# Kernel optimization log

Measured on AMD Instinct MI355X. Metric: run time of the kernel, lower is better.

Reference implementation:

```python
import jax, jax.numpy as jnp
import numpy as np

T, B, N, D, H = 12, 32, 64, 2, 128
HID, HEAD = 32, 4          # GATBlock n_hid, n_head; HEAD*HID == H
M = N * (N - 1)            # edge rows per get_graph
N_ACT = N - 1              # active nodes per batch row


def _make_graph():
    rec = np.zeros((M, N), np.float32)
    snd = np.zeros((M, N), np.float32)
    k = np.arange(N_ACT * N_ACT)
    ii = np.repeat(np.arange(N_ACT), N_ACT)
    jj = np.tile(np.arange(N_ACT), N_ACT)
    snd[k, ii] = 1.0
    rec[k, jj] = 1.0
    return rec, snd


def setup_inputs() -> dict:
    key = jax.random.key(0)
    ks = jax.random.split(key, 16)
    rec, snd = _make_graph()
    inp = {
        "inputs": jax.random.normal(ks[0], (T, B, N, D), jnp.float32),
        "hidden": jax.random.normal(ks[1], (B, N, H), jnp.float32),
        "rel_rec": jnp.asarray(np.broadcast_to(rec, (B, M, N)).copy()),
        "rel_send": jnp.asarray(np.broadcast_to(snd, (B, M, N)).copy()),
        # GATBlock rn1: fc1(D->HID), fc2(2*HID->HEAD)
        "rn1_W1": jax.random.normal(ks[2], (HID, D)) * 0.1,
        "rn1_b1": jnp.zeros((HID,)),
        "rn1_W2": jax.random.normal(ks[3], (HEAD, 2 * HID)) * 0.1,
        "rn1_b2": jnp.zeros((HEAD,)),
        # GATBlock rn2: fc1(H->HID), fc2(2*HID->HEAD)
        "rn2_W1": jax.random.normal(ks[4], (HID, H)) * 0.1,
        "rn2_b1": jnp.zeros((HID,)),
        "rn2_W2": jax.random.normal(ks[5], (HEAD, 2 * HID)) * 0.1,
        "rn2_b2": jnp.zeros((HEAD,)),
        # GRUCell(H, H)
        "gru_Wih": jax.random.normal(ks[6], (3 * H, H)) * 0.05,
        "gru_Whh": jax.random.normal(ks[7], (3 * H, H)) * 0.05,
        "gru_bih": jnp.zeros((3 * H,)),
        "gru_bhh": jnp.zeros((3 * H,)),
        # out Linear(H, D)
        "out_W": jax.random.normal(ks[8], (D, H)) * 0.1,
        "out_b": jnp.zeros((D,)),
    }
    return inp


def _gat_block(x_in, rel_rec, rel_send, W1, b1, W2, b2):
    # x_in: B x N x Din
    x = x_in @ W1.T + b1                                   # B,N,HID
    s = jnp.einsum('bmn,bnd->bmd', rel_send, x)            # B,M,HID (senders)
    r = jnp.einsum('bmn,bnd->bmd', rel_rec, x)             # B,M,HID (receivers)
    a = jax.nn.elu(jnp.concatenate([s, r], -1) @ W2.T + b2)  # B,M,HEAD
    # per-receiving-node masked softmax over the edge dim (edge2node)
    m = rel_rec[..., None] > 0                             # B,M,N,1
    logits = jnp.where(m, a[:, :, None, :], -jnp.inf)      # B,M,N,HEAD
    mx = jnp.max(logits, axis=1, keepdims=True)
    mx = jnp.where(jnp.isfinite(mx), mx, 0.0)
    e = jnp.where(m, jnp.exp(logits - mx), 0.0)
    denom = jnp.sum(e, axis=1, keepdims=True)
    att = e / jnp.where(denom > 0, denom, 1.0)             # B,M,N,HEAD
    # weighted scatter-sum: outer(att_edge, sender_feat) summed per node
    out = jnp.einsum('bmnh,bmd->bnhd', att, s)             # B,N,HEAD,HID
    Bn, Nn = x_in.shape[0], x_in.shape[1]
    return jax.nn.elu(out.reshape(Bn, Nn, HEAD * HID))     # B,N,H


def _gru_cell(x, h, Wih, Whh, bih, bhh):
    gi = x @ Wih.T + bih
    gh = h @ Whh.T + bhh
    i_r, i_z, i_n = jnp.split(gi, 3, axis=-1)
    h_r, h_z, h_n = jnp.split(gh, 3, axis=-1)
    r = jax.nn.sigmoid(i_r + h_r)
    z = jax.nn.sigmoid(i_z + h_z)
    n = jnp.tanh(i_n + r * h_n)
    return (1.0 - z) * n + z * h


def reference(inputs, hidden, rel_rec, rel_send,
              rn1_W1, rn1_b1, rn1_W2, rn1_b2,
              rn2_W1, rn2_b1, rn2_W2, rn2_b2,
              gru_Wih, gru_Whh, gru_bih, gru_bhh,
              out_W, out_b):
    def step(h, x_t):
        x = _gat_block(x_t, rel_rec, rel_send, rn1_W1, rn1_b1, rn1_W2, rn1_b2)
        h = _gru_cell(x, h, gru_Wih, gru_Whh, gru_bih, gru_bhh)
        h = _gat_block(h, rel_rec, rel_send, rn2_W1, rn2_b1, rn2_W2, rn2_b2)
        return h, None
    h_final, _ = jax.lax.scan(step, hidden, inputs)
    pred = h_final @ out_W.T + out_b                       # B,N,D
    return pred
```

## Files before the change

kernel.cpp:

```cpp
#include <hip/hip_runtime.h>


#define T_   12
#define B_   32
#define N_   64
#define D_   2
#define H_   128
#define HID_ 32
#define HEAD_ 4
#define NA_  63

__device__ __forceinline__ float eluf(float x){ return x>0.f ? x : expm1f(x); }

#define OFF_H    0u
#define OFF_X1   262144u
#define OFF_PS1  1048576u
#define OFF_PR1  1146880u
#define OFF_XG   1245184u
#define OFF_X2   4390912u
#define OFF_PS2  4456448u
#define OFF_PR2  4464640u
#define OFF_WT   OFF_X1
#define OFF_GI   4472832u
#define WS_NEED_A ((4472832ull + 9437184ull) * 4ull)

__global__ void gat1_fc(const float* __restrict__ inp, const float* __restrict__ W1,
                        const float* __restrict__ b1, const float* __restrict__ W2,
                        const float* __restrict__ b2,
                        float* __restrict__ x1_all, float* __restrict__ ps_all,
                        float* __restrict__ pr_all){
  int grp = blockIdx.x;
  int tid = threadIdx.x;
  __shared__ float sx1[N_*HID_];
  __shared__ float sW1[HID_*D_];
  __shared__ float sb1[HID_];
  __shared__ float sW2[HEAD_*2*HID_];
  __shared__ float sxin[N_*D_];
  if(tid < 64)  sW1[tid] = W1[tid];
  if(tid < 32)  sb1[tid] = b1[tid];
  sW2[tid] = W2[tid];
  if(tid < 128) sxin[tid] = inp[grp*N_*D_ + tid];
  __syncthreads();
  for(int o = tid; o < N_*HID_; o += 256){
    int n = o >> 5, k = o & 31;
    float v = sb1[k] + sxin[n*2]*sW1[k*2] + sxin[n*2+1]*sW1[k*2+1];
    sx1[o] = v;
    x1_all[grp*N_*HID_ + o] = v;
  }
  __syncthreads();
  for(int p = tid; p < N_*8; p += 256){
    int n = p >> 3, q = p & 7, hh = q & 3;
    const float* w  = sW2 + hh*64 + ((q < 4) ? 0 : 32);
    const float* xr = sx1 + n*32;
    float acc = (q < 4) ? b2[hh] : 0.f;
    #pragma unroll
    for(int c = 0; c < 32; c++) acc += xr[c]*w[c];
    if(q < 4) ps_all[grp*N_*HEAD_ + n*4 + hh] = acc;
    else      pr_all[grp*N_*HEAD_ + n*4 + hh] = acc;
  }
}

__global__ void prep_wt(const float* __restrict__ Wih, const float* __restrict__ Whh,
                        float* __restrict__ wtb){
  int idx = blockIdx.x*256 + threadIdx.x;
  int k4 = idx / 768, j = idx - k4*768;
  const float* src = (j < 384) ? (Wih + (size_t)j*H_) : (Whh + (size_t)(j-384)*H_);
  ((float4*)wtb)[idx] = ((const float4*)src)[k4];
}

__global__ __launch_bounds__(256) void gat_att_gi(const float* __restrict__ x1,
    const float* __restrict__ ps, const float* __restrict__ pr,
    const float* __restrict__ wtb, float* __restrict__ gi){
  int blk = blockIdx.x, g = blk >> 1, ch = blk & 1, tid = threadIdx.x;
  __shared__ float sX[N_*HID_];
  __shared__ float sPs[N_*HEAD_];
  __shared__ float sPr[N_*HEAD_];
  __shared__ __align__(16) float sxg[N_][H_];
  {
    const float4* xs = (const float4*)(x1 + (size_t)g*(N_*HID_));
    ((float4*)sX)[tid]       = xs[tid];
    ((float4*)sX)[tid + 256] = xs[tid + 256];
    sPs[tid] = ps[g*(N_*HEAD_) + tid];
    sPr[tid] = pr[g*(N_*HEAD_) + tid];
  }
  __syncthreads();
  if(tid < NA_*HEAD_){
    int r = tid, hh = r & 3, j = r >> 2;
    float prv = sPr[r];
    float tmax = -1e30f;
    for(int i = 0; i < NA_; i++) tmax = fmaxf(tmax, sPs[i*4 + hh]);
    float m = eluf(tmax + prv);
    float4 acc[8];
    #pragma unroll
    for(int k = 0; k < 8; k++) acc[k] = make_float4(0.f,0.f,0.f,0.f);
    float s = 0.f;
    #pragma unroll 3
    for(int i = 0; i < NA_; i++){
      float tt = sPs[i*4 + hh] + prv;
      float v = tt > 0.f ? tt : expm1f(tt);
      float p = expf(v - m);
      s += p;
      const float4* sxp = (const float4*)&sX[i*32];
      #pragma unroll
      for(int k = 0; k < 8; k++){
        float4 xv = sxp[k];
        acc[k].x += p*xv.x; acc[k].y += p*xv.y;
        acc[k].z += p*xv.z; acc[k].w += p*xv.w;
      }
    }
    float inv = 1.f/s;
    float4* orow = (float4*)&sxg[j][hh*32];
    #pragma unroll
    for(int k = 0; k < 8; k++){
      float4 o;
      o.x = eluf(acc[k].x*inv); o.y = eluf(acc[k].y*inv);
      o.z = eluf(acc[k].z*inv); o.w = eluf(acc[k].w*inv);
      orow[k] = o;
    }
  } else {
    float4 z4 = make_float4(0.f,0.f,0.f,0.f);
    float4* zp = (float4*)sxg[NA_];
    for(int k = tid - NA_*HEAD_; k < 32; k += 4) zp[k] = z4;
  }
  __syncthreads();
  {
    int c = ch*64 + (tid & 63), rh8 = (tid >> 6) * 8;
    const float4* wt4 = (const float4*)wtb;
    #pragma unroll
    for(int pass = 0; pass < 2; pass++){
      int rbase = pass*32 + rh8;
      float ar[8]={0,0,0,0,0,0,0,0}, az[8]={0,0,0,0,0,0,0,0}, an[8]={0,0,0,0,0,0,0,0};
      #pragma unroll 2
      for(int k4 = 0; k4 < 32; k4++){
        float4 w0 = wt4[k4*768 + c];
        float4 w1 = wt4[k4*768 + 128 + c];
        float4 w2 = wt4[k4*768 + 256 + c];
        #pragma unroll
        for(int rr = 0; rr < 8; rr++){
          float4 xv = ((const float4*)sxg[rbase + rr])[k4];
          ar[rr] += w0.x*xv.x + w0.y*xv.y + w0.z*xv.z + w0.w*xv.w;
          az[rr] += w1.x*xv.x + w1.y*xv.y + w1.z*xv.z + w1.w*xv.w;
          an[rr] += w2.x*xv.x + w2.y*xv.y + w2.z*xv.z + w2.w*xv.w;
        }
      }
      #pragma unroll
      for(int rr = 0; rr < 8; rr++){
        size_t base = (size_t)(g*N_ + rbase + rr)*384;
        gi[base + c]       = ar[rr];
        gi[base + 128 + c] = az[rr];
        gi[base + 256 + c] = an[rr];
      }
    }
  }
}

__global__ __launch_bounds__(256) void gat_att_big2(const float* __restrict__ x1,
    const float* __restrict__ ps, const float* __restrict__ pr,
    float* __restrict__ out){
  int blk = blockIdx.x, g = blk >> 1, dh = blk & 1, tid = threadIdx.x;
  __shared__ float sX[N_*HID_];
  __shared__ float sPs[N_*HEAD_];
  __shared__ float sPr[N_*HEAD_];
  {
    const float4* xs = (const float4*)(x1 + (size_t)g*(N_*HID_));
    ((float4*)sX)[tid]       = xs[tid];
    ((float4*)sX)[tid + 256] = xs[tid + 256];
    sPs[tid] = ps[g*(N_*HEAD_) + tid];
    sPr[tid] = pr[g*(N_*HEAD_) + tid];
  }
  __syncthreads();
  float* outg = out + (size_t)g*(N_*H_);
  if(tid < NA_*HEAD_){
    int r = tid, hh = r & 3;
    float prv = sPr[r];
    float tmax = -1e30f;
    for(int i = 0; i < NA_; i++) tmax = fmaxf(tmax, sPs[i*4 + hh]);
    float m = eluf(tmax + prv);
    float4 acc[4];
    #pragma unroll
    for(int k = 0; k < 4; k++) acc[k] = make_float4(0.f,0.f,0.f,0.f);
    float s = 0.f;
    #pragma unroll 3
    for(int i = 0; i < NA_; i++){
      float tt = sPs[i*4 + hh] + prv;
      float v = tt > 0.f ? tt : expm1f(tt);
      float p = expf(v - m);
      s += p;
      const float4* sxp = (const float4*)&sX[i*32 + dh*16];
      #pragma unroll
      for(int k = 0; k < 4; k++){
        float4 xv = sxp[k];
        acc[k].x += p*xv.x; acc[k].y += p*xv.y;
        acc[k].z += p*xv.z; acc[k].w += p*xv.w;
      }
    }
    float inv = 1.f/s;
    float4* orow = (float4*)(outg + (r>>2)*H_ + hh*32 + dh*16);
    #pragma unroll
    for(int k = 0; k < 4; k++){
      float4 o;
      o.x = eluf(acc[k].x*inv); o.y = eluf(acc[k].y*inv);
      o.z = eluf(acc[k].z*inv); o.w = eluf(acc[k].w*inv);
      orow[k] = o;
    }
  } else {
    int hh = tid - NA_*HEAD_;
    float4 z4 = make_float4(0.f,0.f,0.f,0.f);
    float4* zp = (float4*)(outg + NA_*H_ + hh*32 + dh*16);
    zp[0]=z4; zp[1]=z4; zp[2]=z4; zp[3]=z4;
  }
}

__global__ __launch_bounds__(256) void gru_fc8(
    const float* __restrict__ gi, const float* __restrict__ hidden0, int t0,
    const float* __restrict__ x2prev, const float* __restrict__ psprev,
    const float* __restrict__ prprev,
    const float* __restrict__ wtb,
    const float* __restrict__ bih, const float* __restrict__ bhh,
    const float* __restrict__ W1, const float* __restrict__ b1,
    const float* __restrict__ W2, const float* __restrict__ b2,
    float* __restrict__ x2, float* __restrict__ ps2, float* __restrict__ pr2){
  int tid = threadIdx.x, blk = blockIdx.x;
  int g0 = blk*4, g = blk>>4, jbase = (blk&15)*4;
  __shared__ __align__(16) float sX[N_*HID_];
  __shared__ float sPs[N_*HEAD_];
  __shared__ __align__(16) float sh[4][H_];
  __shared__ __align__(16) float shn[4][H_];
  __shared__ float spart[2][12][H_];
  __shared__ float sx2[4][HID_];

  if(t0){
    if(tid < 128) ((float4*)sh)[tid] = ((const float4*)(hidden0 + (size_t)g0*H_))[tid];
  } else {
    ((float4*)sX)[tid]       = ((const float4*)(x2prev + (size_t)g*(N_*HID_)))[tid];
    ((float4*)sX)[tid + 256] = ((const float4*)(x2prev + (size_t)g*(N_*HID_)))[tid + 256];
    sPs[tid] = psprev[g*(N_*HEAD_) + tid];
  }
  __syncthreads();

  if(!t0){
    int rl = tid >> 4, l16 = tid & 15;
    int hh = rl & 3, jrow = rl >> 2;
    int jl = jbase + jrow;
    float prv = prprev[g*(N_*HEAD_) + jbase*4 + rl];
    float tmax = -1e30f;
    for(int i = 0; i < NA_; i++) tmax = fmaxf(tmax, sPs[i*4 + hh]);
    float m = eluf(tmax + prv);
    float a0 = 0.f, a1 = 0.f, s = 0.f;
    #pragma unroll 3
    for(int i = 0; i < NA_; i++){
      float tt = sPs[i*4 + hh] + prv;
      float v = tt > 0.f ? tt : expm1f(tt);
      float p = expf(v - m);
      s += p;
      const float2 xv = *(const float2*)&sX[i*32 + l16*2];
      a0 += p*xv.x; a1 += p*xv.y;
    }
    float inv = 1.f/s;
    float h0 = (jl == NA_) ? 0.f : eluf(a0*inv);
    float h1 = (jl == NA_) ? 0.f : eluf(a1*inv);
    sh[jrow][hh*32 + l16*2]     = h0;
    sh[jrow][hh*32 + l16*2 + 1] = h1;
  }
  __syncthreads();

  int c = tid & 127, rg = tid >> 7;
  {
    const float4* wt4 = (const float4*)wtb;
    float ar[4] = {0,0,0,0};
    float az[4] = {0,0,0,0};
    float an[4] = {0,0,0,0};
    #pragma unroll
    for(int kk = 0; kk < 16; kk++){
      int k4 = rg*16 + kk;
      const float4* wk = wt4 + (size_t)k4*768 + 384 + c;
      float4 wr_ = wk[0], wz_ = wk[128], wn_ = wk[256];
      #pragma unroll
      for(int r = 0; r < 4; r++){
        float4 hv = ((const float4*)sh[r])[k4];
        ar[r] += wr_.x*hv.x + wr_.y*hv.y + wr_.z*hv.z + wr_.w*hv.w;
        az[r] += wz_.x*hv.x + wz_.y*hv.y + wz_.z*hv.z + wz_.w*hv.w;
        an[r] += wn_.x*hv.x + wn_.y*hv.y + wn_.z*hv.z + wn_.w*hv.w;
      }
    }
    #pragma unroll
    for(int r = 0; r < 4; r++){
      spart[rg][r][c]     = ar[r];
      spart[rg][4 + r][c] = az[r];
      spart[rg][8 + r][c] = an[r];
    }
  }
  __syncthreads();

  {
    float bi_r = bih[c], bi_z = bih[c+H_], bi_n = bih[c+2*H_];
    float bh_r = bhh[c], bh_z = bhh[c+H_], bh_n = bhh[c+2*H_];
    int r0 = rg*2;
    #pragma unroll
    for(int rr = 0; rr < 2; rr++){
      int r = r0 + rr;
      float hr = spart[0][r][c]   + spart[1][r][c]   + bh_r;
      float hz = spart[0][4+r][c] + spart[1][4+r][c] + bh_z;
      float hn = spart[0][8+r][c] + spart[1][8+r][c] + bh_n;
      const float* gir = gi + (size_t)(g0+r)*384;
      float ir  = gir[c]     + bi_r;
      float iz  = gir[c+128] + bi_z;
      float in_ = gir[c+256] + bi_n;
      float rgt = 1.f/(1.f+expf(-(ir+hr)));
      float zgt = 1.f/(1.f+expf(-(iz+hz)));
      float ngt = tanhf(in_ + rgt*hn);
      shn[r][c] = (1.f-zgt)*ngt + zgt*sh[r][c];
    }
  }
  __syncthreads();

  if(tid < 128){
    int r = tid >> 5, jc = tid & 31;
    const float4* wrow = (const float4*)(W1 + (size_t)jc*H_);
    const float4* hnr = (const float4*)shn[r];
    float acc = b1[jc];
    #pragma unroll 8
    for(int k4 = 0; k4 < 32; k4++){
      float4 w = wrow[k4], hv = hnr[k4];
      acc += w.x*hv.x + w.y*hv.y + w.z*hv.z + w.w*hv.w;
    }
    sx2[r][jc] = acc;
    x2[(size_t)(g0+r)*HID_ + jc] = acc;
  }
  __syncthreads();
  if(tid < 32){
    int r = tid >> 3, q = tid & 7, hh = q & 3;
    int base = (q < 4) ? 0 : 32;
    float acc = (q < 4) ? b2[hh] : 0.f;
    #pragma unroll
    for(int cc = 0; cc < 32; cc++) acc += sx2[r][cc]*W2[hh*64 + base + cc];
    if(q < 4) ps2[(g0+r)*HEAD_ + hh] = acc;
    else      pr2[(g0+r)*HEAD_ + hh] = acc;
  }
}

__global__ __launch_bounds__(512) void gru_fc3(
    const float* __restrict__ xg, const float* __restrict__ h,
    const float* __restrict__ wtb,
    const float* __restrict__ bih, const float* __restrict__ bhh,
    const float* __restrict__ W1, const float* __restrict__ b1,
    const float* __restrict__ W2, const float* __restrict__ b2,
    float* __restrict__ x2, float* __restrict__ ps2, float* __restrict__ pr2){
  int tid = threadIdx.x;
  int g0 = blockIdx.x * 8;
  __shared__ __align__(16) float sx[8][H_];
  __shared__ __align__(16) float sh[8][H_];
  __shared__ __align__(16) float shn[8][H_];
  __shared__ float sx2[8][HID_];
  if(tid < 256) ((float4*)sx)[tid]     = ((const float4*)(xg + (size_t)g0*H_))[tid];
  else          ((float4*)sh)[tid-256] = ((const float4*)(h  + (size_t)g0*H_))[tid-256];
  __syncthreads();
  int c = tid & 127, rg = tid >> 7, r0 = rg*2;
  const float4* wt4 = (const float4*)wtb;
  const float4* xr0 = (const float4*)sx[r0];
  const float4* xr1 = (const float4*)sx[r0+1];
  const float4* hp0 = (const float4*)sh[r0];
  const float4* hp1 = (const float4*)sh[r0+1];
  float air[2]={0,0}, aiz[2]={0,0}, ain[2]={0,0};
  float ahr[2]={0,0}, ahz[2]={0,0}, ahn[2]={0,0};
  #pragma unroll 2
  for(int k4 = 0; k4 < 32; k4++){
    const float4* wk = wt4 + k4*768 + c;
    float4 w0 = wk[0],   w1 = wk[128], w2 = wk[256];
    float4 w3 = wk[384], w4 = wk[512], w5 = wk[640];
    float4 xv0 = xr0[k4], xv1 = xr1[k4];
    float4 hv0 = hp0[k4], hv1 = hp1[k4];
    air[0] += w0.x*xv0.x + w0.y*xv0.y + w0.z*xv0.z + w0.w*xv0.w;
    aiz[0] += w1.x*xv0.x + w1.y*xv0.y + w1.z*xv0.z + w1.w*xv0.w;
    ain[0] += w2.x*xv0.x + w2.y*xv0.y + w2.z*xv0.z + w2.w*xv0.w;
    ahr[0] += w3.x*hv0.x + w3.y*hv0.y + w3.z*hv0.z + w3.w*hv0.w;
    ahz[0] += w4.x*hv0.x + w4.y*hv0.y + w4.z*hv0.z + w4.w*hv0.w;
    ahn[0] += w5.x*hv0.x + w5.y*hv0.y + w5.z*hv0.z + w5.w*hv0.w;
    air[1] += w0.x*xv1.x + w0.y*xv1.y + w0.z*xv1.z + w0.w*xv1.w;
    aiz[1] += w1.x*xv1.x + w1.y*xv1.y + w1.z*xv1.z + w1.w*xv1.w;
    ain[1] += w2.x*xv1.x + w2.y*xv1.y + w2.z*xv1.z + w2.w*xv1.w;
    ahr[1] += w3.x*hv1.x + w3.y*hv1.y + w3.z*hv1.z + w3.w*hv1.w;
    ahz[1] += w4.x*hv1.x + w4.y*hv1.y + w4.z*hv1.z + w4.w*hv1.w;
    ahn[1] += w5.x*hv1.x + w5.y*hv1.y + w5.z*hv1.z + w5.w*hv1.w;
  }
  float bi_r = bih[c], bi_z = bih[c+H_], bi_n = bih[c+2*H_];
  float bh_r = bhh[c], bh_z = bhh[c+H_], bh_n = bhh[c+2*H_];
  #pragma unroll
  for(int rr = 0; rr < 2; rr++){
    float ir  = air[rr]+bi_r, iz = aiz[rr]+bi_z, in_ = ain[rr]+bi_n;
    float hr  = ahr[rr]+bh_r, hz = ahz[rr]+bh_z, hn  = ahn[rr]+bh_n;
    float rgt = 1.f/(1.f+expf(-(ir+hr)));
    float zgt = 1.f/(1.f+expf(-(iz+hz)));
    float ngt = tanhf(in_ + rgt*hn);
    shn[r0+rr][c] = (1.f-zgt)*ngt + zgt*sh[r0+rr][c];
  }
  __syncthreads();
  if(tid < 256){
    int r = tid >> 5, jc = tid & 31;
    const float4* wrow = (const float4*)(W1 + (size_t)jc*H_);
    const float4* hnr = (const float4*)shn[r];
    float acc = b1[jc];
    #pragma unroll 8
    for(int k4 = 0; k4 < 32; k4++){
      float4 w = wrow[k4], hv = hnr[k4];
      acc += w.x*hv.x + w.y*hv.y + w.z*hv.z + w.w*hv.w;
    }
    sx2[r][jc] = acc;
    x2[(size_t)(g0+r)*HID_ + jc] = acc;
  }
  __syncthreads();
  if(tid < 64){
    int r = tid >> 3, q = tid & 7, hh = q & 3;
    int base = (q < 4) ? 0 : 32;
    float acc = (q < 4) ? b2[hh] : 0.f;
    #pragma unroll
    for(int cc = 0; cc < 32; cc++) acc += sx2[r][cc]*W2[hh*64 + base + cc];
    if(q < 4) ps2[(g0+r)*HEAD_ + hh] = acc;
    else      pr2[(g0+r)*HEAD_ + hh] = acc;
  }
}

__global__ __launch_bounds__(128) void gat_att_sm(const float* __restrict__ x1,
    const float* __restrict__ ps, const float* __restrict__ pr,
    float* __restrict__ out){
  int bid = blockIdx.x;
  int g = bid >> 3, sub = bid & 7, rh = sub >> 2, dq = sub & 3;
  int tid = threadIdx.x;
  __shared__ float sX[N_*HID_];
  __shared__ float sPs[N_*HEAD_];
  __shared__ float sPr[N_*HEAD_];
  {
    const float4* xs = (const float4*)(x1 + (size_t)g*(N_*HID_));
    #pragma unroll
    for(int k = 0; k < 4; k++) ((float4*)sX)[tid + 128*k] = xs[tid + 128*k];
    sPs[tid]       = ps[g*(N_*HEAD_) + tid];
    sPs[tid + 128] = ps[g*(N_*HEAD_) + tid + 128];
    sPr[tid]       = pr[g*(N_*HEAD_) + tid];
    sPr[tid + 128] = pr[g*(N_*HEAD_) + tid + 128];
  }
  __syncthreads();
  float* outg = out + (size_t)g*(N_*H_);
  if(tid < 126){
    int r = rh*126 + tid;
    int hh = r & 3, j = r >> 2;
    float prv = sPr[r];
    float tmax = -1e30f;
    for(int i = 0; i < NA_; i++) tmax = fmaxf(tmax, sPs[i*4 + hh]);
    float m = eluf(tmax + prv);
    float4 a0 = make_float4(0.f,0.f,0.f,0.f), a1 = a0;
    float s = 0.f;
    #pragma unroll 3
    for(int i = 0; i < NA_; i++){
      float tt = sPs[i*4 + hh] + prv;
      float v = tt > 0.f ? tt : expm1f(tt);
      float p = expf(v - m);
      s += p;
      const float4* sxp = (const float4*)&sX[i*32 + dq*8];
      float4 x0 = sxp[0], x1v = sxp[1];
      a0.x += p*x0.x;  a0.y += p*x0.y;  a0.z += p*x0.z;  a0.w += p*x0.w;
      a1.x += p*x1v.x; a1.y += p*x1v.y; a1.z += p*x1v.z; a1.w += p*x1v.w;
    }
    float inv = 1.f/s;
    float4* orow = (float4*)(outg + (size_t)j*H_ + hh*32 + dq*8);
    float4 o0, o1;
    o0.x = eluf(a0.x*inv); o0.y = eluf(a0.y*inv);
    o0.z = eluf(a0.z*inv); o0.w = eluf(a0.w*inv);
    o1.x = eluf(a1.x*inv); o1.y = eluf(a1.y*inv);
    o1.z = eluf(a1.z*inv); o1.w = eluf(a1.w*inv);
    orow[0] = o0; orow[1] = o1;
  } else if(rh == 1){
    float4 z4 = make_float4(0.f,0.f,0.f,0.f);
    float4* zrow = (float4*)(outg + NA_*H_);
    int base = dq*8 + (tid-126)*4;
    #pragma unroll
    for(int k = 0; k < 4; k++) zrow[base + k] = z4;
  }
}

__global__ void final_k(const float* __restrict__ h, const float* __restrict__ oW,
                        const float* __restrict__ ob, float* __restrict__ out){
  int b = blockIdx.x, tid = threadIdx.x;
  int n = tid >> 1, d = tid & 1;
  const float* hr = h + (size_t)(b*N_ + n)*H_;
  float acc = ob[d];
  #pragma unroll 8
  for(int k = 0; k < H_; k++) acc += hr[k]*oW[d*H_ + k];
  out[(b*N_ + n)*D_ + d] = acc;
}

extern "C" void kernel_launch(void* const* d_in, const int* in_sizes, int n_in,
                              void* d_out, int out_size, void* d_ws, size_t ws_size,
                              hipStream_t stream){
  const float* inputs = (const float*)d_in[0];
  const float* hidden = (const float*)d_in[1];
  const float* rn1_W1 = (const float*)d_in[4];
  const float* rn1_b1 = (const float*)d_in[5];
  const float* rn1_W2 = (const float*)d_in[6];
  const float* rn1_b2 = (const float*)d_in[7];
  const float* rn2_W1 = (const float*)d_in[8];
  const float* rn2_b1 = (const float*)d_in[9];
  const float* rn2_W2 = (const float*)d_in[10];
  const float* rn2_b2 = (const float*)d_in[11];
  const float* gWih   = (const float*)d_in[12];
  const float* gWhh   = (const float*)d_in[13];
  const float* gbih   = (const float*)d_in[14];
  const float* gbhh   = (const float*)d_in[15];
  const float* oW     = (const float*)d_in[16];
  const float* ob     = (const float*)d_in[17];
  float* ws = (float*)d_ws;

  const int use_gi = (ws_size >= WS_NEED_A) ? 1 : 0;

  gat1_fc<<<T_*B_, 256, 0, stream>>>(inputs, rn1_W1, rn1_b1, rn1_W2, rn1_b2,
                                     ws + OFF_X1, ws + OFF_PS1, ws + OFF_PR1);
  float* hb = ws + OFF_H;

  if(use_gi){
    float* wtbp = ws + OFF_XG;
    prep_wt<<<96, 256, 0, stream>>>(gWih, gWhh, wtbp);
    gat_att_gi<<<T_*B_*2, 256, 0, stream>>>(ws + OFF_X1, ws + OFF_PS1, ws + OFF_PR1,
                                            wtbp, ws + OFF_GI);
    float* x2b[2] = {ws + OFF_X2,  ws + OFF_PS1};
    float* psb[2] = {ws + OFF_PS2, ws + OFF_PR1};
    float* prb[2] = {ws + OFF_PR2, ws + OFF_PR1 + 8192};
    for(int t = 0; t < T_; t++){
      int w = t & 1, rp = w ^ 1;
      gru_fc8<<<B_*N_/4, 256, 0, stream>>>(ws + OFF_GI + (size_t)t*B_*N_*384,
                                           hidden, (t == 0) ? 1 : 0,
                                           x2b[rp], psb[rp], prb[rp],
                                           wtbp, gbih, gbhh,
                                           rn2_W1, rn2_b1, rn2_W2, rn2_b2,
                                           x2b[w], psb[w], prb[w]);
    }
    gat_att_sm<<<B_*8, 128, 0, stream>>>(x2b[1], psb[1], prb[1], hb);
  } else {
    gat_att_big2<<<T_*B_*2, 256, 0, stream>>>(ws + OFF_X1, ws + OFF_PS1, ws + OFF_PR1,
                                              ws + OFF_XG);
    prep_wt<<<96, 256, 0, stream>>>(gWih, gWhh, ws + OFF_WT);
    const float* xg0  = ws + OFF_XG;
    const float* wtbp = ws + OFF_WT;
    float* x2p = ws + OFF_X2;
    float* psp = ws + OFF_PS2;
    float* prp = ws + OFF_PR2;
    for(int t = 0; t < T_; t++){
      const float* hsrc = (t == 0) ? hidden : hb;
      gru_fc3<<<B_*N_/8, 512, 0, stream>>>(xg0 + (size_t)t*B_*N_*H_, hsrc,
                                           wtbp, gbih, gbhh,
                                           rn2_W1, rn2_b1, rn2_W2, rn2_b2,
                                           x2p, psp, prp);
      gat_att_sm<<<B_*8, 128, 0, stream>>>(x2p, psp, prp, hb);
    }
  }
  final_k<<<B_, 128, 0, stream>>>(hb, oW, ob, (float*)d_out);
}
```

Measured before the change: 469.3 us.

## Split gat_att_gi work by node half instead of gate-column half

Each of the two blocks per graph now computes attention for only its 32 receiving nodes, with the 256 threads splitting the 32 feature dims in halves. Previously both blocks recomputed the full 63-node attention and split only the GRU input-projection columns. The block then computes all 128 gate columns for its 32 rows, removing the duplicated attention work. The shared xg tile is halved and padded to 132 columns to cut bank conflicts, at the cost of each block reading the full weight matrix instead of half.

```diff
diff --git a/kernel.cpp b/kernel.cpp
--- a/kernel.cpp
+++ b/kernel.cpp
@@ -6,6 +6,7 @@
 #define N_   64
 #define D_   2
 #define H_   128
+#define HP_  132
 #define HID_ 32
 #define HEAD_ 4
 #define NA_  63
@@ -68,14 +69,14 @@
   ((float4*)wtb)[idx] = ((const float4*)src)[k4];
 }
 
-__global__ __launch_bounds__(256) void gat_att_gi(const float* __restrict__ x1,
+__global__ __launch_bounds__(256) void gat_att_gi2(const float* __restrict__ x1,
     const float* __restrict__ ps, const float* __restrict__ pr,
     const float* __restrict__ wtb, float* __restrict__ gi){
   int blk = blockIdx.x, g = blk >> 1, ch = blk & 1, tid = threadIdx.x;
   __shared__ float sX[N_*HID_];
   __shared__ float sPs[N_*HEAD_];
   __shared__ float sPr[N_*HEAD_];
-  __shared__ __align__(16) float sxg[N_][H_];
+  __shared__ __align__(16) float sxg[32][HP_];
   {
     const float4* xs = (const float4*)(x1 + (size_t)g*(N_*HID_));
     ((float4*)sX)[tid]       = xs[tid];
@@ -84,15 +85,17 @@
     sPr[tid] = pr[g*(N_*HEAD_) + tid];
   }
   __syncthreads();
-  if(tid < NA_*HEAD_){
-    int r = tid, hh = r & 3, j = r >> 2;
-    float prv = sPr[r];
+  {
+    int r16 = tid & 127, dh = tid >> 7;
+    int jloc = r16 >> 2, hh = r16 & 3;
+    int jl = ch*32 + jloc;
+    float prv = sPr[jl*4 + hh];
     float tmax = -1e30f;
     for(int i = 0; i < NA_; i++) tmax = fmaxf(tmax, sPs[i*4 + hh]);
     float m = eluf(tmax + prv);
-    float4 acc[8];
-    #pragma unroll
-    for(int k = 0; k < 8; k++) acc[k] = make_float4(0.f,0.f,0.f,0.f);
+    float4 acc[4];
+    #pragma unroll
+    for(int k = 0; k < 4; k++) acc[k] = make_float4(0.f,0.f,0.f,0.f);
     float s = 0.f;
     #pragma unroll 3
     for(int i = 0; i < NA_; i++){
@@ -100,35 +103,36 @@
       float v = tt > 0.f ? tt : expm1f(tt);
       float p = expf(v - m);
       s += p;
-      const float4* sxp = (const float4*)&sX[i*32];
+      const float4* sxp = (const float4*)&sX[i*32 + dh*16];
       #pragma unroll
-      for(int k = 0; k < 8; k++){
+      for(int k = 0; k < 4; k++){
         float4 xv = sxp[k];
         acc[k].x += p*xv.x; acc[k].y += p*xv.y;
         acc[k].z += p*xv.z; acc[k].w += p*xv.w;
       }
     }
     float inv = 1.f/s;
-    float4* orow = (float4*)&sxg[j][hh*32];
-    #pragma unroll
-    for(int k = 0; k < 8; k++){
-      float4 o;
-      o.x = eluf(acc[k].x*inv); o.y = eluf(acc[k].y*inv);
-      o.z = eluf(acc[k].z*inv); o.w = eluf(acc[k].w*inv);
-      orow[k] = o;
-    }
-  } else {
-    float4 z4 = make_float4(0.f,0.f,0.f,0.f);
-    float4* zp = (float4*)sxg[NA_];
-    for(int k = tid - NA_*HEAD_; k < 32; k += 4) zp[k] = z4;
-  }
-  __syncthreads();
-  {
-    int c = ch*64 + (tid & 63), rh8 = (tid >> 6) * 8;
+    float4* orow = (float4*)&sxg[jloc][hh*32 + dh*16];
+    if(jl == NA_){
+      float4 z4 = make_float4(0.f,0.f,0.f,0.f);
+      orow[0]=z4; orow[1]=z4; orow[2]=z4; orow[3]=z4;
+    } else {
+      #pragma unroll
+      for(int k = 0; k < 4; k++){
+        float4 o;
+        o.x = eluf(acc[k].x*inv); o.y = eluf(acc[k].y*inv);
+        o.z = eluf(acc[k].z*inv); o.w = eluf(acc[k].w*inv);
+        orow[k] = o;
+      }
+    }
+  }
+  __syncthreads();
+  {
+    int c = tid & 127, rh2 = tid >> 7;
     const float4* wt4 = (const float4*)wtb;
     #pragma unroll
     for(int pass = 0; pass < 2; pass++){
-      int rbase = pass*32 + rh8;
+      int rbase = rh2*16 + pass*8;
       float ar[8]={0,0,0,0,0,0,0,0}, az[8]={0,0,0,0,0,0,0,0}, an[8]={0,0,0,0,0,0,0,0};
       #pragma unroll 2
       for(int k4 = 0; k4 < 32; k4++){
@@ -145,7 +149,7 @@
       }
       #pragma unroll
       for(int rr = 0; rr < 8; rr++){
-        size_t base = (size_t)(g*N_ + rbase + rr)*384;
+        size_t base = (size_t)(g*N_ + ch*32 + rbase + rr)*384;
         gi[base + c]       = ar[rr];
         gi[base + 128 + c] = az[rr];
         gi[base + 256 + c] = an[rr];
@@ -518,8 +522,8 @@
   if(use_gi){
     float* wtbp = ws + OFF_XG;
     prep_wt<<<96, 256, 0, stream>>>(gWih, gWhh, wtbp);
-    gat_att_gi<<<T_*B_*2, 256, 0, stream>>>(ws + OFF_X1, ws + OFF_PS1, ws + OFF_PR1,
-                                            wtbp, ws + OFF_GI);
+    gat_att_gi2<<<T_*B_*2, 256, 0, stream>>>(ws + OFF_X1, ws + OFF_PS1, ws + OFF_PR1,
+                                             wtbp, ws + OFF_GI);
     float* x2b[2] = {ws + OFF_X2,  ws + OFF_PS1};
     float* psb[2] = {ws + OFF_PS2, ws + OFF_PR1};
     float* prb[2] = {ws + OFF_PR2, ws + OFF_PR1 + 8192};
```

Result: no change. 469.4 us (+0.0%).
